# Performance work log

Measured on AMD Instinct MI355X. Metric: run time of the kernel, lower is better.

## Reference

```python
import jax, jax.numpy as jnp
import numpy as np

MODEL_DIM = 1024
NUM_HEADS = 16
HEAD_DIM = MODEL_DIM // NUM_HEADS
BATCH = 2
SEQ = 2048


def setup_inputs() -> dict:
    key = jax.random.key(0)
    k1, k2, k3 = jax.random.split(key, 3)
    scale = 1.0 / np.sqrt(MODEL_DIM)
    return {
        "embeddings": jax.random.normal(k1, (BATCH, SEQ, MODEL_DIM), dtype=jnp.float32),
        "w_qkv": jax.random.normal(k2, (MODEL_DIM, 3 * MODEL_DIM), dtype=jnp.float32) * scale,
        "b_qkv": jnp.zeros((3 * MODEL_DIM,), dtype=jnp.float32),
        "w_out": jax.random.normal(k3, (MODEL_DIM, MODEL_DIM), dtype=jnp.float32) * scale,
        "b_out": jnp.zeros((MODEL_DIM,), dtype=jnp.float32),
    }


def reference(embeddings, w_qkv, b_qkv, w_out, b_out):
    B, S, _ = embeddings.shape
    # fused QKV projection: [B, S, 3*model_dim]
    qkv = embeddings @ w_qkv + b_qkv
    # -> [B, H, S, 3*head_dim], then split
    qkv = qkv.reshape(B, S, NUM_HEADS, 3 * HEAD_DIM).transpose(0, 2, 1, 3)
    q, k, v = jnp.split(qkv, 3, axis=-1)
    # scaled dot-product attention (full O(S^2) matrix, as in original)
    scale = 1.0 / jnp.sqrt(jnp.asarray(HEAD_DIM, dtype=embeddings.dtype))
    scores = jnp.einsum("bhqd,bhkd->bhqk", q, k) * scale
    attn = jax.nn.softmax(scores, axis=-1)
    ctx = jnp.einsum("bhqk,bhkd->bhqd", attn, v)
    # merge heads -> [B, S, model_dim], output projection
    ctx = ctx.transpose(0, 2, 1, 3).reshape(B, S, NUM_HEADS * HEAD_DIM)
    return ctx @ w_out + b_out
```

## Files before the change

kernel.cpp:

```cpp
#include <hip/hip_runtime.h>
#include <hip/hip_bf16.h>

#define MODEL 1024
#define NHEADS 16
#define HDIM 64
#define BATCH 2
#define SEQ 2048
#define NROWS (BATCH*SEQ)
#define QKVN (3*MODEL)
#define QSCALE 0.1803368801111204f

typedef __bf16 bf16x8 __attribute__((ext_vector_type(8)));
typedef float f32x4 __attribute__((ext_vector_type(4)));
typedef float f32x16 __attribute__((ext_vector_type(16)));

#define GLDS(g, l) __builtin_amdgcn_global_load_lds( \
    (const __attribute__((address_space(1))) void*)(g), \
    (__attribute__((address_space(3))) void*)(l), 16, 0, 0)

__device__ inline unsigned cvtpk(float lo, float hi) {
    unsigned r;
    asm("v_cvt_pk_bf16_f32 %0, %1, %2" : "=v"(r) : "v"(lo), "v"(hi));
    return r;
}

__device__ inline size_t qk_fidx(int s, int d) {
    return (((size_t)((s >> 6) * 8 + ((s >> 5) & 1) * 4 + (d >> 4)) * 64)
            + (s & 31) + ((d >> 3) & 1) * 32) * 8 + (d & 7);
}
__device__ inline size_t v_fidx(int s, int d) {
    return (((size_t)((s >> 6) * 8 + (d >> 5) * 4 + ((s >> 4) & 3)) * 64)
            + (d & 31) + ((s >> 3) & 1) * 32) * 8 + (s & 7);
}


__global__ __launch_bounds__(256) void prep_kernel(
    const float* __restrict__ emb, __hip_bfloat16* __restrict__ Xb,
    const float* __restrict__ wqkv, __hip_bfloat16* __restrict__ Wqkvt,
    const float* __restrict__ wout, __hip_bfloat16* __restrict__ Woutt)
{
    __shared__ float tile[32][33];
    int bid = blockIdx.x, tid = threadIdx.x;
    if (bid < 4096) {
        int i = (bid * 256 + tid) * 4;
        float4 v = *(const float4*)(emb + i);
        Xb[i + 0] = __float2bfloat16(v.x);
        Xb[i + 1] = __float2bfloat16(v.y);
        Xb[i + 2] = __float2bfloat16(v.z);
        Xb[i + 3] = __float2bfloat16(v.w);
        return;
    }
    const float* in; __hip_bfloat16* out; int K, N, n0, k0;
    if (bid < 7168) {
        int t = bid - 4096; in = wqkv; out = Wqkvt; K = MODEL; N = QKVN;
        n0 = (t % 96) * 32; k0 = (t / 96) * 32;
    } else {
        int t = bid - 7168; in = wout; out = Woutt; K = MODEL; N = MODEL;
        n0 = (t & 31) * 32; k0 = (t >> 5) * 32;
    }
    int tx = tid & 31, ty = tid >> 5;
#pragma unroll
    for (int i = 0; i < 4; ++i)
        tile[ty + i * 8][tx] = in[(size_t)(k0 + ty + i * 8) * N + n0 + tx];
    __syncthreads();
#pragma unroll
    for (int i = 0; i < 4; ++i)
        out[(size_t)(n0 + ty + i * 8) * K + k0 + tx] = __float2bfloat16(tile[tx][ty + i * 8]);
}


template<int EPI>
__global__ __launch_bounds__(256) void gemm_bt_kernel(
    const __hip_bfloat16* __restrict__ A, const __hip_bfloat16* __restrict__ Bt,
    const float* __restrict__ bias, float* __restrict__ Cf,
    __hip_bfloat16* __restrict__ qb, __hip_bfloat16* __restrict__ kb,
    __hip_bfloat16* __restrict__ vb, int M, int N, int K)
{
    __shared__ __hip_bfloat16 As[128 * 32];
    __shared__ __hip_bfloat16 Bs[128 * 32];
    int tid = threadIdx.x;
    int lane = tid & 63, wv = tid >> 6;
    int wm = wv >> 1, wn = wv & 1;
    int g = lane >> 4, li = lane & 15;
    int row0 = blockIdx.y * 128, col0 = blockIdx.x * 128;

    f32x4 acc[4][4] = {};

    for (int kt = 0; kt < K; kt += 32) {
        __syncthreads();
#pragma unroll
        for (int s = 0; s < 2; ++s) {
            int idx = (s * 256 + tid) * 8;
            int r = idx >> 5, c = idx & 31;
            const __hip_bfloat16* ga = A + (size_t)(row0 + r) * K + kt + c;
            char* la = (char*)As + (size_t)(s * 4 + wv) * 1024;
            GLDS(ga, la);
            const __hip_bfloat16* gb = Bt + (size_t)(col0 + r) * K + kt + c;
            char* lb = (char*)Bs + (size_t)(s * 4 + wv) * 1024;
            GLDS(gb, lb);
        }
        __syncthreads();
        bf16x8 a[4], b[4];
#pragma unroll
        for (int m = 0; m < 4; ++m)
            a[m] = *(const bf16x8*)((const char*)As + (size_t)((wm * 64 + m * 16 + li) * 32 + g * 8) * 2);
#pragma unroll
        for (int n = 0; n < 4; ++n)
            b[n] = *(const bf16x8*)((const char*)Bs + (size_t)((wn * 64 + n * 16 + li) * 32 + g * 8) * 2);
#pragma unroll
        for (int m = 0; m < 4; ++m)
#pragma unroll
            for (int n = 0; n < 4; ++n)
                acc[m][n] = __builtin_amdgcn_mfma_f32_16x16x32_bf16(a[m], b[n], acc[m][n], 0, 0, 0);
    }

    if (EPI == 1) {
#pragma unroll
        for (int m = 0; m < 4; ++m) {
            int row = row0 + wm * 64 + m * 16 + g * 4;
#pragma unroll
            for (int n = 0; n < 4; ++n) {
                int col = col0 + wn * 64 + n * 16 + li;
                float bv = bias[col];
#pragma unroll
                for (int r = 0; r < 4; ++r)
                    Cf[(size_t)(row + r) * N + col] = acc[m][n][r] + bv;
            }
        }
    } else {
#pragma unroll
        for (int m = 0; m < 4; ++m)
#pragma unroll
            for (int r = 0; r < 4; ++r) {
                int row = row0 + wm * 64 + m * 16 + g * 4 + r;
                int b = row >> 11, s = row & 2047;
#pragma unroll
                for (int n = 0; n < 4; ++n) {
                    int col = col0 + wn * 64 + n * 16 + li;
                    float val = acc[m][n][r] + bias[col];
                    int h = col / 192;
                    int rem = col - h * 192;
                    int t = rem >> 6, d = rem & 63;
                    size_t base = (size_t)(b * NHEADS + h) * (SEQ * HDIM);
                    if (t == 0)
                        qb[base + qk_fidx(s, d)] = __float2bfloat16(val * QSCALE);
                    else if (t == 1)
                        kb[base + qk_fidx(s, d)] = __float2bfloat16(val);
                    else
                        vb[base + v_fidx(s, d)] = __float2bfloat16(val);
                }
            }
    }
}


__global__ __launch_bounds__(256, 3) void attn_kernel(
    const __hip_bfloat16* __restrict__ qfb, const __hip_bfloat16* __restrict__ kfb,
    const __hip_bfloat16* __restrict__ vfb, __hip_bfloat16* __restrict__ ctx)
{
    __shared__ float Ms[2][64], Ls[2][64], Os[2][32][64];
    int tid = threadIdx.x;
    int lane = tid & 63, w = tid >> 6;
    int qg = w & 1, kvh = w >> 1;
    int qi = lane & 31, hi = lane >> 5;
    int bh = blockIdx.x;
    int b = bh >> 4, h = bh & 15;
    int q0 = blockIdx.y * 64 + qg * 32;

    const bf16x8* QF = (const bf16x8*)qfb + (size_t)bh * 16384;
    const bf16x8* KF = (const bf16x8*)kfb + (size_t)bh * 16384;
    const bf16x8* VF = (const bf16x8*)vfb + (size_t)bh * 16384;

    bf16x8 qv[4];
#pragma unroll
    for (int st = 0; st < 4; ++st)
        qv[st] = QF[(size_t)blockIdx.y * 512 + (qg * 4 + st) * 64 + lane];

    f32x16 o0 = {}, o1 = {};
    float m = -INFINITY, l = 0.f;

    for (int tt = 0; tt < 16; ++tt) {
        int t = kvh * 16 + tt;
        __builtin_amdgcn_s_barrier();
        bf16x8 kc[8];
#pragma unroll
        for (int f = 0; f < 8; ++f) kc[f] = KF[(size_t)t * 512 + f * 64 + lane];

        f32x16 s0 = {}, s1 = {};
#pragma unroll
        for (int st = 0; st < 4; ++st) {
            s0 = __builtin_amdgcn_mfma_f32_32x32x16_bf16(kc[st], qv[st], s0, 0, 0, 0);
            s1 = __builtin_amdgcn_mfma_f32_32x32x16_bf16(kc[4 + st], qv[st], s1, 0, 0, 0);
        }

        bf16x8 vv[8];
#pragma unroll
        for (int f = 0; f < 8; ++f) vv[f] = VF[(size_t)t * 512 + f * 64 + lane];

        float tm[8];
#pragma unroll
        for (int i = 0; i < 8; ++i)
            tm[i] = fmaxf(fmaxf(s0[i], s0[8 + i]), fmaxf(s1[i], s1[8 + i]));
#pragma unroll
        for (int i = 0; i < 4; ++i) tm[i] = fmaxf(tm[i], tm[4 + i]);
        float mx = fmaxf(fmaxf(tm[0], tm[1]), fmaxf(tm[2], tm[3]));
        mx = fmaxf(mx, __shfl_xor(mx, 32));
        if (__any(mx - m > 8.0f)) {
            float mn = fmaxf(m, mx);
            float al = __builtin_amdgcn_exp2f(m - mn);
            m = mn;
            l *= al;
#pragma unroll
            for (int i = 0; i < 16; ++i) { o0[i] *= al; o1[i] *= al; }
        }
#pragma unroll
        for (int i = 0; i < 16; ++i) s0[i] = __builtin_amdgcn_exp2f(s0[i] - m);
#pragma unroll
        for (int i = 0; i < 16; ++i) s1[i] = __builtin_amdgcn_exp2f(s1[i] - m);
        float ts[8];
#pragma unroll
        for (int i = 0; i < 8; ++i) ts[i] = (s0[i] + s0[8 + i]) + (s1[i] + s1[8 + i]);
#pragma unroll
        for (int i = 0; i < 4; ++i) ts[i] = ts[i] + ts[4 + i];
        float sum = (ts[0] + ts[1]) + (ts[2] + ts[3]);
        sum += __shfl_xor(sum, 32);
        l += sum;

        bf16x8 pb[4];
#pragma unroll
        for (int ks = 0; ks < 4; ++ks) {
            const f32x16& sv = (ks < 2) ? s0 : s1;
            const int base = (ks & 1) * 8;
            unsigned t0 = cvtpk(sv[base + 0], sv[base + 1]);
            unsigned t1 = cvtpk(sv[base + 2], sv[base + 3]);
            unsigned u0 = cvtpk(sv[base + 4], sv[base + 5]);
            unsigned u1 = cvtpk(sv[base + 6], sv[base + 7]);
            unsigned ra = __shfl_xor(hi ? t0 : u0, 32);
            unsigned rb = __shfl_xor(hi ? t1 : u1, 32);
            union { unsigned u[4]; bf16x8 v; } pk;
            pk.u[0] = hi ? ra : t0;
            pk.u[1] = hi ? rb : t1;
            pk.u[2] = hi ? u0 : ra;
            pk.u[3] = hi ? u1 : rb;
            pb[ks] = pk.v;
        }

#pragma unroll
        for (int ks = 0; ks < 4; ++ks) {
            o0 = __builtin_amdgcn_mfma_f32_32x32x16_bf16(vv[ks], pb[ks], o0, 0, 0, 0);
            o1 = __builtin_amdgcn_mfma_f32_32x32x16_bf16(vv[4 + ks], pb[ks], o1, 0, 0, 0);
        }
    }

    __syncthreads();
    if (kvh == 1) {
        Ms[qg][lane] = m; Ls[qg][lane] = l;
#pragma unroll
        for (int i = 0; i < 16; ++i) { Os[qg][i][lane] = o0[i]; Os[qg][16 + i][lane] = o1[i]; }
    }
    __syncthreads();
    if (kvh == 0) {
        float m2 = Ms[qg][lane], l2 = Ls[qg][lane];
        float mn = fmaxf(m, m2);
        float a = __builtin_amdgcn_exp2f(m - mn);
        float b2 = __builtin_amdgcn_exp2f(m2 - mn);
        float linv = 1.f / (l * a + l2 * b2);
        __hip_bfloat16* crow = ctx + ((size_t)(b * SEQ) + q0 + qi) * MODEL + h * HDIM;
#pragma unroll
        for (int rg = 0; rg < 4; ++rg) {
            float c0[4], c1[4];
#pragma unroll
            for (int e = 0; e < 4; ++e) {
                int i = rg * 4 + e;
                c0[e] = (o0[i] * a + Os[qg][i][lane] * b2) * linv;
                c1[e] = (o1[i] * a + Os[qg][16 + i][lane] * b2) * linv;
            }
            uint2 pk0, pk1;
            pk0.x = cvtpk(c0[0], c0[1]); pk0.y = cvtpk(c0[2], c0[3]);
            pk1.x = cvtpk(c1[0], c1[1]); pk1.y = cvtpk(c1[2], c1[3]);
            *(uint2*)(crow + rg * 8 + hi * 4) = pk0;
            *(uint2*)(crow + 32 + rg * 8 + hi * 4) = pk1;
        }
    }
}


extern "C" void kernel_launch(void* const* d_in, const int* in_sizes, int n_in,
                              void* d_out, int out_size, void* d_ws, size_t ws_size,
                              hipStream_t stream) {
    const float* emb = (const float*)d_in[0];
    const float* w_qkv = (const float*)d_in[1];
    const float* b_qkv = (const float*)d_in[2];
    const float* w_out = (const float*)d_in[3];
    const float* b_out = (const float*)d_in[4];
    float* out = (float*)d_out;
    char* ws = (char*)d_ws;

    __hip_bfloat16* Xb    = (__hip_bfloat16*)(ws);
    __hip_bfloat16* Wqkvt = (__hip_bfloat16*)(ws + ((size_t)8  << 20));
    __hip_bfloat16* Woutt = (__hip_bfloat16*)(ws + ((size_t)14 << 20));
    __hip_bfloat16* qbuf  = (__hip_bfloat16*)(ws + ((size_t)16 << 20));
    __hip_bfloat16* kbuf  = (__hip_bfloat16*)(ws + ((size_t)24 << 20));
    __hip_bfloat16* vbuf  = (__hip_bfloat16*)(ws + ((size_t)32 << 20));
    __hip_bfloat16* ctx   = (__hip_bfloat16*)(ws + ((size_t)40 << 20));

    prep_kernel<<<8192, 256, 0, stream>>>(emb, Xb, w_qkv, Wqkvt, w_out, Woutt);

    gemm_bt_kernel<0><<<dim3(QKVN / 128, NROWS / 128), 256, 0, stream>>>(
        Xb, Wqkvt, b_qkv, nullptr, qbuf, kbuf, vbuf, NROWS, QKVN, MODEL);

    attn_kernel<<<dim3(BATCH * NHEADS, SEQ / 64), 256, 0, stream>>>(qbuf, kbuf, vbuf, ctx);

    gemm_bt_kernel<1><<<dim3(MODEL / 128, NROWS / 128), 256, 0, stream>>>(
        ctx, Woutt, b_out, out, nullptr, nullptr, nullptr, NROWS, MODEL, MODEL);
}
```

Measured before the change: 211.4 us.

## Halve attention KV tile to 32 keys, prefetch next K tile, raise occupancy

The attention inner loop now handles 32 keys per iteration instead of 64. It uses one score accumulator instead of two and prefetches the next K fragments into registers while the current tile's softmax and PV run. Launch bounds go from 3 to 4 blocks per CU, which relies on the smaller per-iteration register footprint. In exchange there are twice as many loop iterations, and with them more barriers, max/sum reductions and shuffles per key.

```diff
diff --git a/kernel.cpp b/kernel.cpp
--- a/kernel.cpp
+++ b/kernel.cpp
@@ -154,7 +154,7 @@
 }
 
 
-__global__ __launch_bounds__(256, 3) void attn_kernel(
+__global__ __launch_bounds__(256, 4) void attn_kernel(
     const __hip_bfloat16* __restrict__ qfb, const __hip_bfloat16* __restrict__ kfb,
     const __hip_bfloat16* __restrict__ vfb, __hip_bfloat16* __restrict__ ctx)
 {
@@ -179,28 +179,41 @@
     f32x16 o0 = {}, o1 = {};
     float m = -INFINITY, l = 0.f;
 
-    for (int tt = 0; tt < 16; ++tt) {
-        int t = kvh * 16 + tt;
+    bf16x8 kc[4], kn[4];
+    {
+        int t32 = kvh * 32, t64 = t32 >> 1, rh = t32 & 1;
+#pragma unroll
+        for (int st = 0; st < 4; ++st)
+            kc[st] = KF[(size_t)t64 * 512 + (rh * 4 + st) * 64 + lane];
+    }
+
+    for (int tt = 0; tt < 32; ++tt) {
+        int t32 = kvh * 32 + tt;
+        int t64 = t32 >> 1, rh = t32 & 1;
         __builtin_amdgcn_s_barrier();
-        bf16x8 kc[8];
-#pragma unroll
-        for (int f = 0; f < 8; ++f) kc[f] = KF[(size_t)t * 512 + f * 64 + lane];
-
-        f32x16 s0 = {}, s1 = {};
-#pragma unroll
-        for (int st = 0; st < 4; ++st) {
-            s0 = __builtin_amdgcn_mfma_f32_32x32x16_bf16(kc[st], qv[st], s0, 0, 0, 0);
-            s1 = __builtin_amdgcn_mfma_f32_32x32x16_bf16(kc[4 + st], qv[st], s1, 0, 0, 0);
-        }
-
-        bf16x8 vv[8];
-#pragma unroll
-        for (int f = 0; f < 8; ++f) vv[f] = VF[(size_t)t * 512 + f * 64 + lane];
+
+        f32x16 s = {};
+#pragma unroll
+        for (int st = 0; st < 4; ++st)
+            s = __builtin_amdgcn_mfma_f32_32x32x16_bf16(kc[st], qv[st], s, 0, 0, 0);
+
+        bf16x8 vv[4];
+#pragma unroll
+        for (int dr = 0; dr < 2; ++dr)
+#pragma unroll
+            for (int ksl = 0; ksl < 2; ++ksl)
+                vv[dr * 2 + ksl] = VF[(size_t)t64 * 512 + (dr * 4 + rh * 2 + ksl) * 64 + lane];
+        {
+            int tp = (tt < 31) ? t32 + 1 : t32;
+            int p64 = tp >> 1, ph = tp & 1;
+#pragma unroll
+            for (int st = 0; st < 4; ++st)
+                kn[st] = KF[(size_t)p64 * 512 + (ph * 4 + st) * 64 + lane];
+        }
 
         float tm[8];
 #pragma unroll
-        for (int i = 0; i < 8; ++i)
-            tm[i] = fmaxf(fmaxf(s0[i], s0[8 + i]), fmaxf(s1[i], s1[8 + i]));
+        for (int i = 0; i < 8; ++i) tm[i] = fmaxf(s[i], s[8 + i]);
 #pragma unroll
         for (int i = 0; i < 4; ++i) tm[i] = fmaxf(tm[i], tm[4 + i]);
         float mx = fmaxf(fmaxf(tm[0], tm[1]), fmaxf(tm[2], tm[3]));
@@ -214,27 +227,24 @@
             for (int i = 0; i < 16; ++i) { o0[i] *= al; o1[i] *= al; }
         }
 #pragma unroll
-        for (int i = 0; i < 16; ++i) s0[i] = __builtin_amdgcn_exp2f(s0[i] - m);
-#pragma unroll
-        for (int i = 0; i < 16; ++i) s1[i] = __builtin_amdgcn_exp2f(s1[i] - m);
+        for (int i = 0; i < 16; ++i) s[i] = __builtin_amdgcn_exp2f(s[i] - m);
         float ts[8];
 #pragma unroll
-        for (int i = 0; i < 8; ++i) ts[i] = (s0[i] + s0[8 + i]) + (s1[i] + s1[8 + i]);
+        for (int i = 0; i < 8; ++i) ts[i] = s[i] + s[8 + i];
 #pragma unroll
         for (int i = 0; i < 4; ++i) ts[i] = ts[i] + ts[4 + i];
         float sum = (ts[0] + ts[1]) + (ts[2] + ts[3]);
         sum += __shfl_xor(sum, 32);
         l += sum;
 
-        bf16x8 pb[4];
-#pragma unroll
-        for (int ks = 0; ks < 4; ++ks) {
-            const f32x16& sv = (ks < 2) ? s0 : s1;
-            const int base = (ks & 1) * 8;
-            unsigned t0 = cvtpk(sv[base + 0], sv[base + 1]);
-            unsigned t1 = cvtpk(sv[base + 2], sv[base + 3]);
-            unsigned u0 = cvtpk(sv[base + 4], sv[base + 5]);
-            unsigned u1 = cvtpk(sv[base + 6], sv[base + 7]);
+        bf16x8 pb[2];
+#pragma unroll
+        for (int ksl = 0; ksl < 2; ++ksl) {
+            const int base = ksl * 8;
+            unsigned t0 = cvtpk(s[base + 0], s[base + 1]);
+            unsigned t1 = cvtpk(s[base + 2], s[base + 3]);
+            unsigned u0 = cvtpk(s[base + 4], s[base + 5]);
+            unsigned u1 = cvtpk(s[base + 6], s[base + 7]);
             unsigned ra = __shfl_xor(hi ? t0 : u0, 32);
             unsigned rb = __shfl_xor(hi ? t1 : u1, 32);
             union { unsigned u[4]; bf16x8 v; } pk;
@@ -242,14 +252,16 @@
             pk.u[1] = hi ? rb : t1;
             pk.u[2] = hi ? u0 : ra;
             pk.u[3] = hi ? u1 : rb;
-            pb[ks] = pk.v;
-        }
-
-#pragma unroll
-        for (int ks = 0; ks < 4; ++ks) {
-            o0 = __builtin_amdgcn_mfma_f32_32x32x16_bf16(vv[ks], pb[ks], o0, 0, 0, 0);
-            o1 = __builtin_amdgcn_mfma_f32_32x32x16_bf16(vv[4 + ks], pb[ks], o1, 0, 0, 0);
-        }
+            pb[ksl] = pk.v;
+        }
+
+        o0 = __builtin_amdgcn_mfma_f32_32x32x16_bf16(vv[0], pb[0], o0, 0, 0, 0);
+        o0 = __builtin_amdgcn_mfma_f32_32x32x16_bf16(vv[1], pb[1], o0, 0, 0, 0);
+        o1 = __builtin_amdgcn_mfma_f32_32x32x16_bf16(vv[2], pb[0], o1, 0, 0, 0);
+        o1 = __builtin_amdgcn_mfma_f32_32x32x16_bf16(vv[3], pb[1], o1, 0, 0, 0);
+
+#pragma unroll
+        for (int st = 0; st < 4; ++st) kc[st] = kn[st];
     }
 
     __syncthreads();
```

Measured after the change: 206.8 us. -2.1%, faster.
